# Kernel tuning notes

Hardware: AMD Instinct MI355X
Metric: run time of the kernel (lower is better)

## Reference

```python
import jax, jax.numpy as jnp
import numpy as np


def hard_sig(x):
    # Keras hard_sigmoid: relu6(x + 3) / 6
    return jnp.clip(x / 6.0 + 0.5, 0.0, 1.0)


def conv2d(x, k):
    # x: (B,H,W,Cin), k: (kh,kw,Cin,Cout), SAME padding, stride 1
    return jax.lax.conv_general_dilated(x, k, (1, 1), 'SAME',
                                        dimension_numbers=('NHWC', 'HWIO', 'NHWC'))


def convlstm_layer(xs, Wk, Uk, b):
    # xs: (B,T,H,W,Cin); Wk: (kh,kw,Cin,4F); Uk: (kh,kw,F,4F); b: (4F,)
    B, T, H, W, _ = xs.shape
    F = b.shape[0] // 4
    h0 = jnp.zeros((B, H, W, F), xs.dtype)
    c0 = jnp.zeros((B, H, W, F), xs.dtype)
    xs_t = jnp.moveaxis(xs, 1, 0)  # (T,B,H,W,Cin)

    def step(carry, xt):
        h, c = carry
        z = conv2d(xt, Wk) + conv2d(h, Uk) + b
        zi, zf, zg, zo = jnp.split(z, 4, axis=-1)  # Keras gate order i,f,c,o
        i = hard_sig(zi)
        f = hard_sig(zf)
        o = hard_sig(zo)
        c_new = f * c + i * jax.nn.relu(zg)      # activation='relu'
        h_new = o * jax.nn.relu(c_new)
        return (h_new, c_new), h_new

    _, hs = jax.lax.scan(step, (h0, c0), xs_t)
    return jnp.moveaxis(hs, 0, 1)  # (B,T,H,W,F)


def batchnorm(x, gamma, beta, mean, var):
    # inference-mode BN over last axis, keras eps=1e-3
    return (x - mean) * jax.lax.rsqrt(var + 1e-3) * gamma + beta


def maxpool_hw(x):
    # MaxPooling3D pool_size=(1,2,2), SAME, channels_last; x: (B,T,H,W,C)
    return jax.lax.reduce_window(x, -jnp.inf, jax.lax.max,
                                 (1, 1, 2, 2, 1), (1, 1, 2, 2, 1), 'SAME')


def setup_inputs() -> dict:
    key = jax.random.key(0)
    ks = jax.random.split(key, 16)
    s = 0.1
    F = 32
    inp = {
        'x': jax.random.normal(ks[0], (16, 16, 64, 64, 1), jnp.float32),
        'k1': jax.random.normal(ks[1], (5, 5, 1, 4 * F), jnp.float32) * s,
        'u1': jax.random.normal(ks[2], (5, 5, F, 4 * F), jnp.float32) * s,
        'b1': jnp.zeros((4 * F,), jnp.float32),
        'g1': jnp.ones((F,), jnp.float32),
        'be1': jnp.zeros((F,), jnp.float32),
        'm1': jnp.zeros((F,), jnp.float32),
        'v1': jnp.ones((F,), jnp.float32),
        'k2': jax.random.normal(ks[3], (5, 5, F, 4 * F), jnp.float32) * s,
        'u2': jax.random.normal(ks[4], (5, 5, F, 4 * F), jnp.float32) * s,
        'b2': jnp.zeros((4 * F,), jnp.float32),
        'g2': jnp.ones((F,), jnp.float32),
        'be2': jnp.zeros((F,), jnp.float32),
        'm2': jnp.zeros((F,), jnp.float32),
        'v2': jnp.ones((F,), jnp.float32),
        'k3': jax.random.normal(ks[5], (3, 3, F, 4 * F), jnp.float32) * s,
        'u3': jax.random.normal(ks[6], (3, 3, F, 4 * F), jnp.float32) * s,
        'b3': jnp.zeros((4 * F,), jnp.float32),
        'wd': jax.random.normal(ks[7], (F, 64 * 64), jnp.float32) * s,
        'bd': jnp.zeros((64 * 64,), jnp.float32),
    }
    return inp


def reference(x, k1, u1, b1, g1, be1, m1, v1,
              k2, u2, b2, g2, be2, m2, v2,
              k3, u3, b3, wd, bd):
    h = convlstm_layer(x, k1, u1, b1)
    h = batchnorm(h, g1, be1, m1, v1)
    h = maxpool_hw(h)  # (B,T,32,32,32)
    h = convlstm_layer(h, k2, u2, b2)
    h = batchnorm(h, g2, be2, m2, v2)
    h = maxpool_hw(h)  # (B,T,16,16,32)
    h = convlstm_layer(h, k3, u3, b3)
    gap = jnp.mean(h, axis=(1, 2, 3))  # GlobalAveragePooling3D -> (B,32)
    logits = gap @ wd + bd
    return jax.nn.softmax(logits, axis=-1)
```

## Files before the change

kernel.cpp:

```cpp
#include <hip/hip_runtime.h>

typedef unsigned short u16;
typedef unsigned int u32;
typedef __attribute__((ext_vector_type(8))) short bf16x8;
typedef __attribute__((ext_vector_type(4))) float f32x4;

__device__ __forceinline__ float b2f(u16 h) {
  union { float f; unsigned u; } v; v.u = ((unsigned)h) << 16; return v.f;
}
__device__ __forceinline__ u16 f2b(float f) {
  union { float f; unsigned u; } v; v.f = f;
  unsigned r = v.u + 0x7fffu + ((v.u >> 16) & 1u);
  return (u16)(r >> 16);
}
__device__ __forceinline__ float hsig(float z) {
  return fminf(fmaxf(z * 0.16666667f + 0.5f, 0.f), 1.f);
}
__device__ __forceinline__ float ldf(const void* p, int i, int flag) {
  return flag ? b2f(((const u16*)p)[i]) : ((const float*)p)[i];
}

__global__ void detect_dtype(const void* x, int* dflag) {
  __shared__ int cnt;
  if (threadIdx.x == 0) cnt = 0;
  __syncthreads();
  const u32* w = (const u32*)x;
  int c = 0;
  for (int i = threadIdx.x; i < 512; i += 256) {
    u32 e = (w[i] >> 7) & 0xFFu;
    if (e >= 100 && e < 130) c++;
  }
  atomicAdd(&cnt, c);
  __syncthreads();
  if (threadIdx.x == 0) *dflag = (cnt >= 256) ? 1 : 0;
}

__global__ void canon_x(const void* src, u16* dst, const int* dflag, int n) {
  int i = blockIdx.x * 256 + threadIdx.x;
  if (i >= n) return;
  int fl = *dflag;
  float v = ldf(src, i, fl);
  u16 hi = f2b(v);
  dst[i] = hi;
  dst[i + n] = f2b(v - b2f(hi));
}

template<int KS, int MODE, int H, int W, int MROWS>
__device__ __forceinline__
void step_body(int bxi, int b, char* dsm,
               const u16* __restrict__ src, int aBStride, size_t sPL,
               const u16* __restrict__ wA, const u16* __restrict__ wU,
               const u16* __restrict__ hin, size_t hPL, u16* __restrict__ hout,
               float* __restrict__ cbuf, const void* __restrict__ bias,
               const void* __restrict__ bng, const void* __restrict__ bnb,
               const void* __restrict__ bnm, const void* __restrict__ bnv,
               u16* __restrict__ pooled, size_t pPL, float* __restrict__ gap,
               const int* __restrict__ dflag)
{
  constexpr int PAD = KS / 2;
  constexpr int TW = 8 + 2 * PAD;
  constexpr int TH = MROWS + 2 * PAD;
  constexpr int KK = KS * KS;
  constexpr int KT = (MODE == 0) ? (KK + 1) : (2 * KK);
  constexpr int MT = MROWS / 4;
  constexpr int NPX = TH * TW;
  constexpr int BUFSZ = NPX * 32;
  constexpr int ASZ0 = (NPX + 15) & ~15;

  u16* sH0 = (u16*)dsm;
  u16* sH1 = sH0 + BUFSZ;
  u16* sA0 = sH1 + BUFSZ;
  u16* sA1 = sA0 + ((MODE == 0) ? ASZ0 : BUFSZ);
  float* sgap = (float*)(sA1 + ((MODE == 0) ? ASZ0 : BUFSZ));

  const int tid = threadIdx.x;
  constexpr int TXT = W / 8;
  const int bx0 = (bxi % TXT) * 8;
  const int gy0 = (bxi / TXT) * MROWS;

  const int w = tid >> 6, lane = tid & 63;
  const int j = w & 1, R0 = (w >> 1) * (MROWS / 2);
  const int q = lane >> 4, col = lane & 15;
  const int my = (lane >> 3) & 1, mx = lane & 7;

  if (MODE == 2 && tid < 32) sgap[tid] = 0.f;

  auto swadr = [](int px, int c) {
    return (px << 5) + (((c ^ px ^ (px >> 1)) & 3) << 3);
  };

  auto stageH = [&](int pl, u16* dst) {
    const u16* hsrc = hin + (size_t)pl * hPL;
    for (int i = tid; i < NPX * 4; i += 256) {
      int p = i >> 2, ch = i & 3;
      int sy = p / TW, sx = p - sy * TW;
      int gy = gy0 + sy - PAD, gx = bx0 + sx - PAD;
      int4 v; v.x = v.y = v.z = v.w = 0;
      if (gy >= 0 && gy < H && gx >= 0 && gx < W)
        v = *(const int4*)(hsrc + (((size_t)(b * H + gy) * W + gx) << 5) + ch * 8);
      *(int4*)(&dst[swadr(p, ch)]) = v;
    }
  };
  auto stageS = [&](int pl, u16* dst) {
    const u16* asrc = src + (size_t)pl * sPL;
    if (MODE == 0) {
      for (int i = tid; i < NPX; i += 256) {
        int sy = i / TW, sx = i - sy * TW;
        int gy = gy0 + sy - PAD, gx = bx0 + sx - PAD;
        u16 v = 0;
        if (gy >= 0 && gy < H && gx >= 0 && gx < W)
          v = asrc[(size_t)b * aBStride + gy * W + gx];
        dst[i] = v;
      }
    } else {
      for (int i = tid; i < NPX * 4; i += 256) {
        int p = i >> 2, ch = i & 3;
        int sy = p / TW, sx = p - sy * TW;
        int gy = gy0 + sy - PAD, gx = bx0 + sx - PAD;
        int4 v; v.x = v.y = v.z = v.w = 0;
        if (gy >= 0 && gy < H && gx >= 0 && gx < W)
          v = *(const int4*)(asrc + (size_t)b * aBStride + (((size_t)gy * W + gx) << 5) + ch * 8);
        *(int4*)(&dst[swadr(p, ch)]) = v;
      }
    }
  };

  const int wfoff = lane * 8;
  auto loadW = [&](int kt, bf16x8* dst) {
    const u16* wsrc;
    if (MODE == 0) wsrc = (kt == 0) ? wA : (wU + (kt - 1) * 4096);
    else           wsrc = (kt < KK) ? (wA + kt * 4096) : (wU + (kt - KK) * 4096);
#pragma unroll
    for (int g = 0; g < 4; g++)
      dst[g] = *(const bf16x8*)(wsrc + ((j + 2 * g) * 64) * 8 + wfoff);
  };

  f32x4 acc[MT][4] = {};
  int pxb[MT];
#pragma unroll
  for (int mt = 0; mt < MT; mt++)
    pxb[mt] = (R0 + 2 * mt + my) * TW + mx;

  stageH(0, sH0); stageH(1, sH1); stageS(0, sA0); stageS(1, sA1);
  __syncthreads();

  bf16x8 bw[4];
  loadW(0, bw);
#pragma unroll 2
  for (int kt = 0; kt < KT; ++kt) {
    bf16x8 nxt[4];
    if (kt + 1 < KT) loadW(kt + 1, nxt);
    bf16x8 ah[MT], al[MT];
    if (MODE == 0 && kt == 0) {
#pragma unroll
      for (int mt = 0; mt < MT; mt++) {
        union { bf16x8 v; u16 e[8]; } uh, ul;
#pragma unroll
        for (int jj = 0; jj < 8; jj++) {
          int k = q * 8 + jj;
          u16 vh = 0, vl = 0;
          if (k < KK) {
            int kh = k / KS, kw = k - kh * KS;
            int o = (R0 + 2 * mt + my + kh) * TW + (mx + kw);
            vh = sA0[o]; vl = sA1[o];
          }
          uh.e[jj] = vh; ul.e[jj] = vl;
        }
        ah[mt] = uh.v; al[mt] = ul.v;
      }
    } else {
      int tap; const u16 *s0, *s1;
      if (MODE == 0)    { tap = kt - 1;  s0 = sH0; s1 = sH1; }
      else if (kt < KK) { tap = kt;      s0 = sA0; s1 = sA1; }
      else              { tap = kt - KK; s0 = sH0; s1 = sH1; }
      const int koff = (tap / KS) * TW + (tap - (tap / KS) * KS);
#pragma unroll
      for (int mt = 0; mt < MT; mt++) {
        const int px = pxb[mt] + koff;
        const int ad = (px << 5) + (((q ^ px ^ (px >> 1)) & 3) << 3);
        ah[mt] = *(const bf16x8*)(s0 + ad);
        al[mt] = *(const bf16x8*)(s1 + ad);
      }
    }
#pragma unroll
    for (int mt = 0; mt < MT; mt++)
#pragma unroll
      for (int g = 0; g < 4; g++)
        acc[mt][g] = __builtin_amdgcn_mfma_f32_16x16x32_bf16(ah[mt], bw[g], acc[mt][g], 0, 0, 0);
#pragma unroll
    for (int mt = 0; mt < MT; mt++)
#pragma unroll
      for (int g = 0; g < 4; g++)
        acc[mt][g] = __builtin_amdgcn_mfma_f32_16x16x32_bf16(al[mt], bw[g], acc[mt][g], 0, 0, 0);
#pragma unroll
    for (int g = 0; g < 4; g++) bw[g] = nxt[g];
  }

  const int fl = *dflag;
  const int f = j * 16 + col;
  const float bi  = ldf(bias, f, fl);
  const float bff = ldf(bias, 32 + f, fl);
  const float bg  = ldf(bias, 64 + f, fl);
  const float bo  = ldf(bias, 96 + f, fl);
  float sc = 0.f, sh = 0.f;
  if (MODE < 2) {
    sc = ldf(bng, f, fl) * rsqrtf(ldf(bnv, f, fl) + 1e-3f);
    sh = ldf(bnb, f, fl) - ldf(bnm, f, fl) * sc;
  }
  const int oy = q >> 1;
  const int ox = (q & 1) * 4;
  float gsum = 0.f;
#pragma unroll
  for (int mt = 0; mt < MT; mt++) {
    const int y = gy0 + R0 + 2 * mt + oy;
    const size_t base = (((size_t)(b * H + y) * W + (bx0 + ox)) << 5) + f;
    float bnp[4];
#pragma unroll
    for (int r = 0; r < 4; r++) {
      float zi = acc[mt][0][r] + bi;
      float zf = acc[mt][1][r] + bff;
      float zg = acc[mt][2][r] + bg;
      float zo = acc[mt][3][r] + bo;
      float ig = hsig(zi), fg = hsig(zf), og = hsig(zo);
      float gg = fmaxf(zg, 0.f);
      size_t idx = base + ((size_t)r << 5);
      float cold = cbuf[idx];
      float cn = fg * cold + ig * gg;
      cbuf[idx] = cn;
      float hn = og * fmaxf(cn, 0.f);
      u16 hhi = f2b(hn);
      hout[idx] = hhi;
      hout[idx + hPL] = f2b(hn - b2f(hhi));
      if (MODE < 2) bnp[r] = hn * sc + sh; else gsum += hn;
    }
    if (MODE < 2) {
      float p0 = fmaxf(bnp[0], bnp[1]);
      float p1 = fmaxf(bnp[2], bnp[3]);
      p0 = fmaxf(p0, __shfl_xor(p0, 32));
      p1 = fmaxf(p1, __shfl_xor(p1, 32));
      if (q < 2) {
        const int py = (gy0 + R0 + 2 * mt) >> 1;
        const int px = (bx0 >> 1) + (q & 1) * 2;
        size_t pb = (((size_t)(b * (H / 2) + py) * (W / 2) + px) << 5) + f;
        u16 phi = f2b(p0);
        pooled[pb] = phi;
        pooled[pb + pPL] = f2b(p0 - b2f(phi));
        u16 qhi = f2b(p1);
        pooled[pb + 32] = qhi;
        pooled[pb + 32 + pPL] = f2b(p1 - b2f(qhi));
      }
    }
  }
  if (MODE == 2) {
    atomicAdd(&sgap[f], gsum);
    __syncthreads();
    if (tid < 32) atomicAdd(&gap[b * 32 + tid], sgap[tid]);
  }
}

__global__ __launch_bounds__(256, 3)
void fused_step(int t, const u16* __restrict__ xc,
                const u16* __restrict__ W1x, const u16* __restrict__ W1u,
                u16* h1a, u16* h1b, float* c1, const void* b1, const void* g1,
                const void* be1, const void* m1, const void* v1, u16* p1,
                const u16* __restrict__ W2k, const u16* __restrict__ W2u,
                u16* h2a, u16* h2b, float* c2, const void* b2, const void* g2,
                const void* be2, const void* m2, const void* v2, u16* p2,
                const u16* __restrict__ W3k, const u16* __restrict__ W3u,
                u16* h3a, u16* h3b, float* c3, const void* b3,
                float* gap, const int* dflag)
{
  extern __shared__ char dsm[];
  const int grp = blockIdx.x / 25;
  const int r   = blockIdx.x % 25;
  if (r < 16) {
    if (t > 15) return;
    const int idx = grp * 16 + r;
    const u16* h1i = (t & 1) ? h1b : h1a; u16* h1o = (t & 1) ? h1a : h1b;
    step_body<5, 0, 64, 64, 16>(idx & 31, idx >> 5, dsm,
        xc + (size_t)t * 4096, 65536, 1048576, W1x, W1u, h1i, 2097152, h1o, c1,
        b1, g1, be1, m1, v1, p1 + (size_t)(t & 1) * 1048576, 524288, nullptr, dflag);
  } else if (r < 24) {
    const int tt = t - 1; if (tt < 0 || tt > 15) return;
    const int idx = grp * 8 + (r - 16);
    const u16* h2i = (tt & 1) ? h2b : h2a; u16* h2o = (tt & 1) ? h2a : h2b;
    step_body<5, 1, 32, 32, 8>(idx & 15, idx >> 4, dsm,
        p1 + (size_t)(tt & 1) * 1048576, 32768, 524288, W2k, W2u, h2i, 524288, h2o, c2,
        b2, g2, be2, m2, v2, p2 + (size_t)(tt & 1) * 262144, 131072, nullptr, dflag);
  } else {
    const int tt = t - 2; if (tt < 0 || tt > 15) return;
    const int idx = grp;
    const u16* h3i = (tt & 1) ? h3b : h3a; u16* h3o = (tt & 1) ? h3a : h3b;
    step_body<3, 2, 16, 16, 16>(idx & 1, idx >> 1, dsm,
        p2 + (size_t)(tt & 1) * 262144, 8192, 131072, W3k, W3u, h3i, 131072, h3o, c3,
        b3, nullptr, nullptr, nullptr, nullptr, nullptr, 0, gap, dflag);
  }
}

__global__ void repack_w(const void* __restrict__ src, u16* __restrict__ dst,
                         int taps, const int* __restrict__ dflag) {
  int i = blockIdx.x * 256 + threadIdx.x;
  if (i >= taps * 512) return;
  int fl = *dflag;
  int l = i & 63, nt = (i >> 6) & 7, tap = i >> 9;
  int q = l >> 4, col = l & 15;
  u16 tmp[8];
#pragma unroll
  for (int j = 0; j < 8; j++)
    tmp[j] = f2b(ldf(src, (tap * 32 + q * 8 + j) * 128 + nt * 16 + col, fl));
#pragma unroll
  for (int j = 0; j < 8; j++) dst[i * 8 + j] = tmp[j];
}
__global__ void repack_x(const void* __restrict__ src, u16* __restrict__ dst,
                         const int* __restrict__ dflag) {
  int i = blockIdx.x * 256 + threadIdx.x;
  if (i >= 512) return;
  int fl = *dflag;
  int l = i & 63, nt = (i >> 6) & 7;
  int q = l >> 4, col = l & 15;
#pragma unroll
  for (int j = 0; j < 8; j++) {
    int k = q * 8 + j;
    dst[i * 8 + j] = (k < 25) ? f2b(ldf(src, k * 128 + nt * 16 + col, fl)) : (u16)0;
  }
}

__global__ void zero_ws(int4* p, int n) {
  int i = blockIdx.x * 256 + threadIdx.x;
  if (i < n) { int4 z; z.x = z.y = z.z = z.w = 0; p[i] = z; }
}
__global__ void fillv(float* out, int n, float v) {
  int i = blockIdx.x * 256 + threadIdx.x;
  if (i < n) out[i] = v;
}

__global__ void logits_k(const float* __restrict__ gap, const void* __restrict__ wd,
                         const void* __restrict__ bd, float* __restrict__ lg,
                         const int* __restrict__ dflag) {
  int i = blockIdx.x * 256 + threadIdx.x;
  int b = i >> 12, o = i & 4095;
  int fl = *dflag;
  float s = ldf(bd, o, fl);
  const float scl = 1.0f / 4096.0f;
#pragma unroll
  for (int f = 0; f < 32; f++)
    s += gap[b * 32 + f] * scl * ldf(wd, f * 4096 + o, fl);
  lg[i] = s;
}

__global__ void softmax_k(const float* __restrict__ lg, float* __restrict__ out) {
  int b = blockIdx.x, tid = threadIdx.x;
  __shared__ float red[256];
  float v[16];
  float lmax = -1e30f;
#pragma unroll
  for (int i = 0; i < 16; i++) {
    v[i] = lg[b * 4096 + i * 256 + tid];
    lmax = fmaxf(lmax, v[i]);
  }
  red[tid] = lmax; __syncthreads();
  for (int st = 128; st > 0; st >>= 1) { if (tid < st) red[tid] = fmaxf(red[tid], red[tid + st]); __syncthreads(); }
  float M = red[0]; __syncthreads();
  float ls = 0.f;
#pragma unroll
  for (int i = 0; i < 16; i++) { v[i] = expf(v[i] - M); ls += v[i]; }
  red[tid] = ls; __syncthreads();
  for (int st = 128; st > 0; st >>= 1) { if (tid < st) red[tid] += red[tid + st]; __syncthreads(); }
  float inv = 1.0f / red[0];
#pragma unroll
  for (int i = 0; i < 16; i++) out[b * 4096 + i * 256 + tid] = v[i] * inv;
}

extern "C" void kernel_launch(void* const* d_in, const int* in_sizes, int n_in,
                              void* d_out, int out_size, void* d_ws, size_t ws_size,
                              hipStream_t stream)
{
  const void* x   = d_in[0];
  const void* k1  = d_in[1];
  const void* u1  = d_in[2];
  const void* b1  = d_in[3];
  const void* g1  = d_in[4];
  const void* be1 = d_in[5];
  const void* m1  = d_in[6];
  const void* v1  = d_in[7];
  const void* k2  = d_in[8];
  const void* u2  = d_in[9];
  const void* b2  = d_in[10];
  const void* g2  = d_in[11];
  const void* be2 = d_in[12];
  const void* m2  = d_in[13];
  const void* v2  = d_in[14];
  const void* k3  = d_in[15];
  const void* u3  = d_in[16];
  const void* b3  = d_in[17];
  const void* wd  = d_in[18];
  const void* bd  = d_in[19];
  float* out = (float*)d_out;

  char* ws = (char*)d_ws;
  size_t off = 0;
  auto alloc = [&](size_t bytes) -> char* {
    char* p = ws + off; off = (off + bytes + 255) & ~(size_t)255; return p;
  };
  float* c1  = (float*)alloc(2097152 * 4);
  float* c2  = (float*)alloc(524288 * 4);
  float* c3  = (float*)alloc(131072 * 4);
  u16*   h1a = (u16*)alloc(2097152 * 2 * 2);
  u16*   h2a = (u16*)alloc(524288 * 2 * 2);
  u16*   h3a = (u16*)alloc(131072 * 2 * 2);
  float* gap = (float*)alloc(512 * 4);
  int*   dflag = (int*)alloc(64);
  size_t zero_bytes = off;
  u16* h1b = (u16*)alloc(2097152 * 2 * 2);
  u16* h2b = (u16*)alloc(524288 * 2 * 2);
  u16* h3b = (u16*)alloc(131072 * 2 * 2);
  u16* p1  = (u16*)alloc(524288 * 2 * 2 * 2);
  u16* p2  = (u16*)alloc(131072 * 2 * 2 * 2);
  u16* xc  = (u16*)alloc(1048576 * 2 * 2);
  float* lgbuf = (float*)alloc(65536 * 4);
  u16* W1x = (u16*)alloc(4096 * 2);
  u16* W1u = (u16*)alloc(102400 * 2);
  u16* W2k = (u16*)alloc(102400 * 2);
  u16* W2u = (u16*)alloc(102400 * 2);
  u16* W3k = (u16*)alloc(36864 * 2);
  u16* W3u = (u16*)alloc(36864 * 2);

  if (ws_size < off) {
    fillv<<<dim3((out_size + 255) / 256), 256, 0, stream>>>(out, out_size, 0.5f);
    return;
  }

  int nz = (int)(zero_bytes / 16);
  zero_ws<<<dim3((nz + 255) / 256), 256, 0, stream>>>((int4*)ws, nz);
  detect_dtype<<<1, 256, 0, stream>>>(x, dflag);
  canon_x<<<4096, 256, 0, stream>>>(x, xc, dflag, 1048576);
  repack_x<<<2, 256, 0, stream>>>(k1, W1x, dflag);
  repack_w<<<50, 256, 0, stream>>>(u1, W1u, 25, dflag);
  repack_w<<<50, 256, 0, stream>>>(k2, W2k, 25, dflag);
  repack_w<<<50, 256, 0, stream>>>(u2, W2u, 25, dflag);
  repack_w<<<18, 256, 0, stream>>>(k3, W3k, 9, dflag);
  repack_w<<<18, 256, 0, stream>>>(u3, W3u, 9, dflag);

  const size_t dyn = 46336;
  for (int t = 0; t < 18; ++t) {
    fused_step<<<800, 256, dyn, stream>>>(t, xc,
        W1x, W1u, h1a, h1b, c1, b1, g1, be1, m1, v1, p1,
        W2k, W2u, h2a, h2b, c2, b2, g2, be2, m2, v2, p2,
        W3k, W3u, h3a, h3b, c3, b3, gap, dflag);
  }
  logits_k<<<256, 256, 0, stream>>>(gap, wd, bd, lgbuf, dflag);
  softmax_k<<<16, 256, 0, stream>>>(lgbuf, out);
}
```

Before: 1.208 ms.

## Stage halo tiles via direct global-to-LDS loads and rebalance layer-3 blocks

Replaces the register round-trip staging of hidden-state and input tiles with global_load_lds 16-byte direct-to-LDS transfers. Out-of-bounds pixels read from a zeroed pad buffer, and the swizzle is applied on the source side. Layer 3 is split into smaller 8-row tiles across twice as many blocks. LDS size drops and the launch bound rises to 4 blocks per CU, aiming for higher occupancy and less staging overhead. The risk is extra register pressure under the tighter launch bound and correctness of the swizzle inversion.

```diff
diff --git a/kernel.cpp b/kernel.cpp
--- a/kernel.cpp
+++ b/kernel.cpp
@@ -18,6 +18,11 @@
 }
 __device__ __forceinline__ float ldf(const void* p, int i, int flag) {
   return flag ? b2f(((const u16*)p)[i]) : ((const float*)p)[i];
+}
+__device__ __forceinline__ void glds16(const void* g, void* l) {
+  __builtin_amdgcn_global_load_lds(
+      (const __attribute__((address_space(1))) void*)g,
+      (__attribute__((address_space(3))) void*)(u32)(size_t)l, 16, 0, 0);
 }
 
 __global__ void detect_dtype(const void* x, int* dflag) {
@@ -47,7 +52,7 @@
 
 template<int KS, int MODE, int H, int W, int MROWS>
 __device__ __forceinline__
-void step_body(int bxi, int b, char* dsm,
+void step_body(int bxi, int b, char* dsm, const u16* __restrict__ zp,
                const u16* __restrict__ src, int aBStride, size_t sPL,
                const u16* __restrict__ wA, const u16* __restrict__ wU,
                const u16* __restrict__ hin, size_t hPL, u16* __restrict__ hout,
@@ -64,14 +69,15 @@
   constexpr int KT = (MODE == 0) ? (KK + 1) : (2 * KK);
   constexpr int MT = MROWS / 4;
   constexpr int NPX = TH * TW;
-  constexpr int BUFSZ = NPX * 32;
+  constexpr int CALLS = (NPX * 32 + 511) / 512;
+  constexpr int BUFP = CALLS * 512;
   constexpr int ASZ0 = (NPX + 15) & ~15;
 
   u16* sH0 = (u16*)dsm;
-  u16* sH1 = sH0 + BUFSZ;
-  u16* sA0 = sH1 + BUFSZ;
-  u16* sA1 = sA0 + ((MODE == 0) ? ASZ0 : BUFSZ);
-  float* sgap = (float*)(sA1 + ((MODE == 0) ? ASZ0 : BUFSZ));
+  u16* sH1 = sH0 + BUFP;
+  u16* sA0 = sH1 + BUFP;
+  u16* sA1 = sA0 + ((MODE == 0) ? ASZ0 : BUFP);
+  float* sgap = (float*)(sA1 + ((MODE == 0) ? ASZ0 : BUFP));
 
   const int tid = threadIdx.x;
   constexpr int TXT = W / 8;
@@ -85,43 +91,29 @@
 
   if (MODE == 2 && tid < 32) sgap[tid] = 0.f;
 
-  auto swadr = [](int px, int c) {
-    return (px << 5) + (((c ^ px ^ (px >> 1)) & 3) << 3);
-  };
-
-  auto stageH = [&](int pl, u16* dst) {
-    const u16* hsrc = hin + (size_t)pl * hPL;
-    for (int i = tid; i < NPX * 4; i += 256) {
-      int p = i >> 2, ch = i & 3;
-      int sy = p / TW, sx = p - sy * TW;
+  auto stageC = [&](const u16* gsrc, u16* dst) {
+    for (int k = w; k < CALLS; k += 4) {
+      int idx = k * 512 + lane * 8;
+      int px = idx >> 5;
+      int slot = (idx >> 3) & 3;
+      int c = (slot ^ px ^ (px >> 1)) & 3;
+      int sy = px / TW, sx = px - sy * TW;
       int gy = gy0 + sy - PAD, gx = bx0 + sx - PAD;
-      int4 v; v.x = v.y = v.z = v.w = 0;
-      if (gy >= 0 && gy < H && gx >= 0 && gx < W)
-        v = *(const int4*)(hsrc + (((size_t)(b * H + gy) * W + gx) << 5) + ch * 8);
-      *(int4*)(&dst[swadr(p, ch)]) = v;
+      const u16* g = zp;
+      if (px < NPX && gy >= 0 && gy < H && gx >= 0 && gx < W)
+        g = gsrc + (((size_t)(b * H + gy) * W + gx) << 5) + c * 8;
+      glds16(g, dst + (size_t)k * 512);
     }
   };
-  auto stageS = [&](int pl, u16* dst) {
+  auto stageX = [&](int pl, u16* dst) {
     const u16* asrc = src + (size_t)pl * sPL;
-    if (MODE == 0) {
-      for (int i = tid; i < NPX; i += 256) {
-        int sy = i / TW, sx = i - sy * TW;
-        int gy = gy0 + sy - PAD, gx = bx0 + sx - PAD;
-        u16 v = 0;
-        if (gy >= 0 && gy < H && gx >= 0 && gx < W)
-          v = asrc[(size_t)b * aBStride + gy * W + gx];
-        dst[i] = v;
-      }
-    } else {
-      for (int i = tid; i < NPX * 4; i += 256) {
-        int p = i >> 2, ch = i & 3;
-        int sy = p / TW, sx = p - sy * TW;
-        int gy = gy0 + sy - PAD, gx = bx0 + sx - PAD;
-        int4 v; v.x = v.y = v.z = v.w = 0;
-        if (gy >= 0 && gy < H && gx >= 0 && gx < W)
-          v = *(const int4*)(asrc + (size_t)b * aBStride + (((size_t)gy * W + gx) << 5) + ch * 8);
-        *(int4*)(&dst[swadr(p, ch)]) = v;
-      }
+    for (int i = tid; i < NPX; i += 256) {
+      int sy = i / TW, sx = i - sy * TW;
+      int gy = gy0 + sy - PAD, gx = bx0 + sx - PAD;
+      u16 v = 0;
+      if (gy >= 0 && gy < H && gx >= 0 && gx < W)
+        v = asrc[(size_t)b * aBStride + gy * W + gx];
+      dst[i] = v;
     }
   };
 
@@ -141,7 +133,10 @@
   for (int mt = 0; mt < MT; mt++)
     pxb[mt] = (R0 + 2 * mt + my) * TW + mx;
 
-  stageH(0, sH0); stageH(1, sH1); stageS(0, sA0); stageS(1, sA1);
+  stageC(hin, sH0);
+  stageC(hin + hPL, sH1);
+  if (MODE == 0) { stageX(0, sA0); stageX(1, sA1); }
+  else           { stageC(src, sA0); stageC(src + sPL, sA1); }
   __syncthreads();
 
   bf16x8 bw[4];
@@ -258,8 +253,8 @@
   }
 }
 
-__global__ __launch_bounds__(256, 3)
-void fused_step(int t, const u16* __restrict__ xc,
+__global__ __launch_bounds__(256, 4)
+void fused_step(int t, const u16* __restrict__ xc, const u16* __restrict__ zp,
                 const u16* __restrict__ W1x, const u16* __restrict__ W1u,
                 u16* h1a, u16* h1b, float* c1, const void* b1, const void* g1,
                 const void* be1, const void* m1, const void* v1, u16* p1,
@@ -271,27 +266,27 @@
                 float* gap, const int* dflag)
 {
   extern __shared__ char dsm[];
-  const int grp = blockIdx.x / 25;
-  const int r   = blockIdx.x % 25;
+  const int grp = blockIdx.x / 26;
+  const int r   = blockIdx.x % 26;
   if (r < 16) {
     if (t > 15) return;
     const int idx = grp * 16 + r;
     const u16* h1i = (t & 1) ? h1b : h1a; u16* h1o = (t & 1) ? h1a : h1b;
-    step_body<5, 0, 64, 64, 16>(idx & 31, idx >> 5, dsm,
+    step_body<5, 0, 64, 64, 16>(idx & 31, idx >> 5, dsm, zp,
         xc + (size_t)t * 4096, 65536, 1048576, W1x, W1u, h1i, 2097152, h1o, c1,
         b1, g1, be1, m1, v1, p1 + (size_t)(t & 1) * 1048576, 524288, nullptr, dflag);
   } else if (r < 24) {
     const int tt = t - 1; if (tt < 0 || tt > 15) return;
     const int idx = grp * 8 + (r - 16);
     const u16* h2i = (tt & 1) ? h2b : h2a; u16* h2o = (tt & 1) ? h2a : h2b;
-    step_body<5, 1, 32, 32, 8>(idx & 15, idx >> 4, dsm,
+    step_body<5, 1, 32, 32, 8>(idx & 15, idx >> 4, dsm, zp,
         p1 + (size_t)(tt & 1) * 1048576, 32768, 524288, W2k, W2u, h2i, 524288, h2o, c2,
         b2, g2, be2, m2, v2, p2 + (size_t)(tt & 1) * 262144, 131072, nullptr, dflag);
   } else {
     const int tt = t - 2; if (tt < 0 || tt > 15) return;
-    const int idx = grp;
+    const int idx = grp * 2 + (r - 24);
     const u16* h3i = (tt & 1) ? h3b : h3a; u16* h3o = (tt & 1) ? h3a : h3b;
-    step_body<3, 2, 16, 16, 16>(idx & 1, idx >> 1, dsm,
+    step_body<3, 2, 16, 16, 8>(idx & 3, idx >> 2, dsm, zp,
         p2 + (size_t)(tt & 1) * 262144, 8192, 131072, W3k, W3u, h3i, 131072, h3o, c3,
         b3, nullptr, nullptr, nullptr, nullptr, nullptr, 0, gap, dflag);
   }
@@ -410,6 +405,7 @@
   u16*   h3a = (u16*)alloc(131072 * 2 * 2);
   float* gap = (float*)alloc(512 * 4);
   int*   dflag = (int*)alloc(64);
+  u16*   zp  = (u16*)alloc(2048);
   size_t zero_bytes = off;
   u16* h1b = (u16*)alloc(2097152 * 2 * 2);
   u16* h2b = (u16*)alloc(524288 * 2 * 2);
@@ -441,9 +437,9 @@
   repack_w<<<18, 256, 0, stream>>>(k3, W3k, 9, dflag);
   repack_w<<<18, 256, 0, stream>>>(u3, W3u, 9, dflag);
 
-  const size_t dyn = 46336;
+  const size_t dyn = 37120;
   for (int t = 0; t < 18; ++t) {
-    fused_step<<<800, 256, dyn, stream>>>(t, xc,
+    fused_step<<<832, 256, dyn, stream>>>(t, xc, zp,
         W1x, W1u, h1a, h1b, c1, b1, g1, be1, m1, v1, p1,
         W2k, W2u, h2a, h2b, c2, b2, g2, be2, m2, v2, p2,
         W3k, W3u, h3a, h3b, c3, b3, gap, dflag);
```

After: 3.349 ms. 2.77x slower.
